# Optimization experiments

Hardware: AMD Instinct MI355X
Metric: run time of the kernel (lower is better)

## Reference

```python
import jax, jax.numpy as jnp
import numpy as np

D_MODEL = 1024
N_HEADS = 16
D_K = D_MODEL // N_HEADS
NEG = -1e9


def setup_inputs() -> dict:
    key = jax.random.key(0)
    ks = jax.random.split(key, 10)
    B, S = 4, 2048
    x = jax.random.normal(ks[0], (B, S, D_MODEL), dtype=jnp.float32)
    mask = jax.random.randint(ks[1], (B, S, S), 0, 2).astype(jnp.bool_)
    sc = 1.0 / np.sqrt(D_MODEL)
    Wq = jax.random.normal(ks[2], (D_MODEL, D_MODEL), dtype=jnp.float32) * sc
    bq = jnp.zeros((D_MODEL,), dtype=jnp.float32)
    Wk = jax.random.normal(ks[3], (D_MODEL, D_MODEL), dtype=jnp.float32) * sc
    bk = jnp.zeros((D_MODEL,), dtype=jnp.float32)
    Wv = jax.random.normal(ks[4], (D_MODEL, D_MODEL), dtype=jnp.float32) * sc
    bv = jnp.zeros((D_MODEL,), dtype=jnp.float32)
    Wo = jax.random.normal(ks[5], (D_MODEL, D_MODEL), dtype=jnp.float32) * sc
    bo = jnp.zeros((D_MODEL,), dtype=jnp.float32)
    return {"x": x, "mask": mask, "Wq": Wq, "bq": bq, "Wk": Wk, "bk": bk,
            "Wv": Wv, "bv": bv, "Wo": Wo, "bo": bo}


def _split_heads(t, B, S):
    # [B,S,d_model] -> [B,H,S,d_k]
    return t.reshape(B, S, N_HEADS, D_K).transpose(0, 2, 1, 3)


def reference(x, mask, Wq, bq, Wk, bk, Wv, bv, Wo, bo):
    B, S, _ = x.shape
    Q = _split_heads(x @ Wq + bq, B, S)
    K = _split_heads(x @ Wk + bk, B, S)
    V = _split_heads(x @ Wv + bv, B, S)
    scale = jnp.sqrt(jnp.float32(D_K))
    scores = jnp.einsum('bhqd,bhkd->bhqk', Q, K) / scale
    scores = jnp.where(mask[:, None, :, :], jnp.float32(NEG), scores)
    attn = jax.nn.softmax(scores, axis=-1)
    ctx = jnp.einsum('bhqk,bhkd->bhqd', attn, V)
    ctx = ctx.transpose(0, 2, 1, 3).reshape(B, S, D_MODEL)
    return ctx @ Wo + bo
```

## Files before the change

kernel.cpp:

```cpp
#include <hip/hip_runtime.h>

#define D_MODEL 1024
#define N_HEADS 16
#define D_K     64
#define BATCH   4
#define SEQ     2048
#define MROWS   (BATCH * SEQ)
#define QSCALE  0.18033688011112042f

typedef __bf16 bf16x8 __attribute__((ext_vector_type(8)));
typedef float  f32x4  __attribute__((ext_vector_type(4)));
typedef float  f32x16 __attribute__((ext_vector_type(16)));
typedef unsigned short ushort8 __attribute__((ext_vector_type(8)));
typedef unsigned short ushort4v __attribute__((ext_vector_type(4)));

#if __has_builtin(__builtin_amdgcn_exp2f)
#define EXP2F(x) __builtin_amdgcn_exp2f(x)
#else
#define EXP2F(x) exp2f(x)
#endif

__device__ inline unsigned short f2bf(float f) {
    union { float f; unsigned int u; } v; v.f = f;
    unsigned int u = v.u;
    unsigned int r = (u + 0x7fffu + ((u >> 16) & 1u)) >> 16;
    return (unsigned short)r;
}

__device__ inline void load_lds16(const void* g, void* l) {
    __builtin_amdgcn_global_load_lds(
        (const __attribute__((address_space(1))) unsigned int*)g,
        (__attribute__((address_space(3))) unsigned int*)l, 16, 0, 0);
}

__global__ __launch_bounds__(256) void wprep(const float* __restrict__ Wq,
                                             const float* __restrict__ Wk,
                                             const float* __restrict__ Wv,
                                             const float* __restrict__ Wo,
                                             unsigned short* __restrict__ wt) {
    __shared__ __align__(16) unsigned short t[64][65];
    int w  = blockIdx.z;
    const float* W = (w == 0) ? Wq : (w == 1) ? Wk : (w == 2) ? Wv : Wo;
    int k0 = blockIdx.x * 64, n0 = blockIdx.y * 64;
    int tid = threadIdx.x;
    int nl = tid & 63, kq = tid >> 6;
#pragma unroll
    for (int i = 0; i < 16; i++) {
        int kl = kq * 16 + i;
        t[kl][nl] = f2bf(W[(size_t)(k0 + kl) * D_MODEL + n0 + nl]);
    }
    __syncthreads();
    unsigned short* out = wt + (size_t)w * D_MODEL * D_MODEL;
#pragma unroll
    for (int p = 0; p < 2; p++) {
        int nrow = p * 32 + (tid >> 3);
        int c8   = (tid & 7) * 8;
        ushort8 o;
#pragma unroll
        for (int j = 0; j < 8; j++) o[j] = t[c8 + j][nrow];
        *reinterpret_cast<ushort8*>(out + (size_t)(n0 + nrow) * D_MODEL + k0 + c8) = o;
    }
}

__global__ __launch_bounds__(256) void xprep(const float4* __restrict__ x,
                                             unsigned short* __restrict__ xb) {
    int i = blockIdx.x * 256 + threadIdx.x;
    float4 v = x[i];
    ushort4v o;
    o[0] = f2bf(v.x); o[1] = f2bf(v.y); o[2] = f2bf(v.z); o[3] = f2bf(v.w);
    *reinterpret_cast<ushort4v*>(xb + (size_t)i * 4) = o;
}

__global__ __launch_bounds__(256) void mprep(const int* __restrict__ mask,
                                             unsigned long long* __restrict__ mb) {
    int row = blockIdx.x;
    int tid = threadIdx.x;
    int wv  = tid >> 6;
#pragma unroll
    for (int w = 0; w < 8; w++) {
        int col = w * 256 + tid;
        int mval = mask[(size_t)row * SEQ + col];
        unsigned long long bits = __ballot(mval != 0);
        if ((tid & 63) == 0) mb[(size_t)row * 32 + w * 4 + wv] = bits;
    }
}

__global__ __launch_bounds__(256) void qkv_gemm(const unsigned short* __restrict__ xb,
                                                const unsigned short* __restrict__ wt,
                                                const float* __restrict__ bq,
                                                const float* __restrict__ bk,
                                                const float* __restrict__ bvv,
                                                unsigned short* __restrict__ qb,
                                                unsigned short* __restrict__ kb,
                                                unsigned short* __restrict__ vt) {
    __shared__ __align__(16) unsigned short lds_a[128 * 32];
    __shared__ __align__(16) unsigned short lds_b[128 * 32];
    int tid = threadIdx.x;
    int wave = tid >> 6, lane = tid & 63;
    int c = lane & 15, g = lane >> 4;
    int wave_m = (wave & 1) * 64, wave_n = (wave >> 1) * 64;
    int nblk = blockIdx.x * 128, mblk = blockIdx.y * 128;

    int oct0 = wave * 128 + lane, oct1 = oct0 + 64;
    int ra0 = oct0 >> 2, ga0 = ((oct0 & 3) ^ (ra0 & 3)) * 8;
    int ra1 = oct1 >> 2, ga1 = ((oct1 & 3) ^ (ra1 & 3)) * 8;
    const unsigned short* pa0 = xb + (size_t)(mblk + ra0) * D_MODEL + ga0;
    const unsigned short* pa1 = xb + (size_t)(mblk + ra1) * D_MODEL + ga1;
    const unsigned short* pb0 = wt + (size_t)(nblk + ra0) * D_MODEL + ga0;
    const unsigned short* pb1 = wt + (size_t)(nblk + ra1) * D_MODEL + ga1;
    unsigned short* la0 = lds_a + wave * 1024;
    unsigned short* la1 = la0 + 512;
    unsigned short* lb0 = lds_b + wave * 1024;
    unsigned short* lb1 = lb0 + 512;

    int aoff[4], boff[4];
#pragma unroll
    for (int mi = 0; mi < 4; mi++) {
        int row = wave_m + mi * 16 + c;
        aoff[mi] = (row * 4 + (g ^ (row & 3))) * 16;
    }
#pragma unroll
    for (int ni = 0; ni < 4; ni++) {
        int row = wave_n + ni * 16 + c;
        boff[ni] = (row * 4 + (g ^ (row & 3))) * 16;
    }

    f32x4 acc[4][4];
#pragma unroll
    for (int mi = 0; mi < 4; mi++)
#pragma unroll
        for (int ni = 0; ni < 4; ni++) acc[mi][ni] = f32x4{0.f, 0.f, 0.f, 0.f};

    for (int k0 = 0; k0 < D_MODEL; k0 += 32) {
        load_lds16(pa0 + k0, la0);
        load_lds16(pa1 + k0, la1);
        load_lds16(pb0 + k0, lb0);
        load_lds16(pb1 + k0, lb1);
        __syncthreads();
        bf16x8 af[4], bfr[4];
#pragma unroll
        for (int mi = 0; mi < 4; mi++)
            af[mi] = *reinterpret_cast<const bf16x8*>(reinterpret_cast<const char*>(lds_a) + aoff[mi]);
#pragma unroll
        for (int ni = 0; ni < 4; ni++)
            bfr[ni] = *reinterpret_cast<const bf16x8*>(reinterpret_cast<const char*>(lds_b) + boff[ni]);
#pragma unroll
        for (int mi = 0; mi < 4; mi++)
#pragma unroll
            for (int ni = 0; ni < 4; ni++)
                acc[mi][ni] = __builtin_amdgcn_mfma_f32_16x16x32_bf16(af[mi], bfr[ni], acc[mi][ni], 0, 0, 0);
        __syncthreads();
    }

    int nb = nblk + wave_n;
    int wsel = nb >> 10;
    int h = (nb >> 6) & 15;
    int dk0 = nb & 63;
    int mglob = mblk + wave_m;
    int b = mglob >> 11;
    int s0 = mglob & (SEQ - 1);
    size_t bh = (size_t)(b * N_HEADS + h);
    const float* bias = (wsel == 0) ? bq : (wsel == 1) ? bk : bvv;
    int nn = nb & (D_MODEL - 1);
    float bval[4];
#pragma unroll
    for (int ni = 0; ni < 4; ni++) bval[ni] = bias[nn + ni * 16 + c];
    float oscale = (wsel == 0) ? QSCALE : 1.0f;

    if (wsel < 2) {
        unsigned short* outp = wsel ? kb : qb;
#pragma unroll
        for (int mi = 0; mi < 4; mi++)
#pragma unroll
            for (int ni = 0; ni < 4; ni++) {
                int dk = dk0 + ni * 16 + c;
#pragma unroll
                for (int r = 0; r < 4; r++) {
                    int s = s0 + mi * 16 + g * 4 + r;
                    outp[(bh * SEQ + s) * 64 + dk] = f2bf((acc[mi][ni][r] + bval[ni]) * oscale);
                }
            }
    } else {
#pragma unroll
        for (int mi = 0; mi < 4; mi++)
#pragma unroll
            for (int ni = 0; ni < 4; ni++) {
                int dk = dk0 + ni * 16 + c;
                int s = s0 + mi * 16 + g * 4;
                ushort4v o;
#pragma unroll
                for (int r = 0; r < 4; r++) o[r] = f2bf(acc[mi][ni][r] + bval[ni]);
                *reinterpret_cast<ushort4v*>(vt + (bh * 64 + dk) * SEQ + s) = o;
            }
    }
}

__global__ __launch_bounds__(128) void attn(const unsigned short* __restrict__ qb,
                                            const unsigned short* __restrict__ kb,
                                            const unsigned short* __restrict__ vt,
                                            const unsigned long long* __restrict__ mb,
                                            unsigned short* __restrict__ ctx) {
    __shared__ __align__(16) unsigned char smem[25088];
    unsigned short* lk = (unsigned short*)smem;
    unsigned short* lv = (unsigned short*)(smem + 8192);
    unsigned int*  lpw = (unsigned int*)(smem + 16384);

    int tid = threadIdx.x;
    int wave = tid >> 6, lane = tid & 63;
    int q31 = lane & 31, hi = lane >> 5;
    int bh = blockIdx.x >> 5;
    int q0 = (blockIdx.x & 31) * 64 + wave * 32;
    int b = bh >> 4, h = bh & 15;
    const unsigned short* qbase = qb + (size_t)bh * SEQ * 64;
    const unsigned short* kbase = kb + (size_t)bh * SEQ * 64;
    const unsigned short* vbase = vt + (size_t)bh * 64 * SEQ;
    const unsigned long long* mp = mb + ((size_t)b * SEQ + q0 + q31) * 32;

    bf16x8 qf[4];
    {
        const unsigned short* qr = qbase + (size_t)(q0 + q31) * 64 + hi * 8;
#pragma unroll
        for (int c = 0; c < 4; c++)
            qf[c] = *reinterpret_cast<const bf16x8*>(qr + c * 16);
    }

    int srow = lane >> 3;
    int soct = (lane & 7) ^ srow;
    const unsigned short* ksrc[4];
    const unsigned short* vsrc[4];
    unsigned short* klb[4];
    unsigned short* vlb[4];
#pragma unroll
    for (int i = 0; i < 4; i++) {
        int rbase = 16 * i + 8 * wave;
        ksrc[i] = kbase + (size_t)(rbase + srow) * 64 + soct * 8;
        vsrc[i] = vbase + (size_t)(rbase + srow) * SEQ + soct * 8;
        klb[i] = lk + rbase * 64;
        vlb[i] = lv + rbase * 64;
    }

    int kofs[2][4];
#pragma unroll
    for (int s = 0; s < 2; s++)
#pragma unroll
        for (int c = 0; c < 4; c++)
            kofs[s][c] = (32 * s + q31) * 128 + (((hi + 2 * c) ^ (q31 & 7)) * 16);

    unsigned int* pw = lpw + wave * 1088 + q31 * 34 + 2 * hi;
    const unsigned int* prd = lpw + wave * 1088 + q31 * 34 + 4 * hi;

    float lsum = 0.f;
    f32x16 po[2];
#pragma unroll
    for (int i = 0; i < 16; i++) { po[0][i] = 0.f; po[1][i] = 0.f; }

    for (int it = 0; it < SEQ / 64; it++) {
#pragma unroll
        for (int i = 0; i < 4; i++) {
            load_lds16(ksrc[i] + it * 4096, klb[i]);
            load_lds16(vsrc[i] + it * 64, vlb[i]);
        }
        unsigned long long w64 = mp[it];
        __syncthreads();

        const char* lkb = (const char*)lk;
        const char* lvb = (const char*)lv;

        f32x16 sq[2];
#pragma unroll
        for (int i = 0; i < 16; i++) { sq[0][i] = 0.f; sq[1][i] = 0.f; }
#pragma unroll
        for (int c = 0; c < 4; c++) {
            sq[0] = __builtin_amdgcn_mfma_f32_32x32x16_bf16(
                *reinterpret_cast<const bf16x8*>(lkb + kofs[0][c]), qf[c], sq[0], 0, 0, 0);
            sq[1] = __builtin_amdgcn_mfma_f32_32x32x16_bf16(
                *reinterpret_cast<const bf16x8*>(lkb + kofs[1][c]), qf[c], sq[1], 0, 0, 0);
        }

#pragma unroll
        for (int s = 0; s < 2; s++) {
            unsigned int wt = ~(unsigned int)(w64 >> (32 * s));
#pragma unroll
            for (int j = 0; j < 4; j++) {
                unsigned int nj = wt >> (8 * j + 4 * hi);
                unsigned int t0, t1, t2, t3;
                {
                    float p = EXP2F(sq[s][4 * j + 0]);
                    unsigned int m = (unsigned int)((int)(nj << 31) >> 31);
                    t0 = __float_as_uint(p) & m; lsum += __uint_as_float(t0);
                }
                {
                    float p = EXP2F(sq[s][4 * j + 1]);
                    unsigned int m = (unsigned int)((int)(nj << 30) >> 31);
                    t1 = __float_as_uint(p) & m; lsum += __uint_as_float(t1);
                }
                {
                    float p = EXP2F(sq[s][4 * j + 2]);
                    unsigned int m = (unsigned int)((int)(nj << 29) >> 31);
                    t2 = __float_as_uint(p) & m; lsum += __uint_as_float(t2);
                }
                {
                    float p = EXP2F(sq[s][4 * j + 3]);
                    unsigned int m = (unsigned int)((int)(nj << 28) >> 31);
                    t3 = __float_as_uint(p) & m; lsum += __uint_as_float(t3);
                }
                uint2 u;
                u.x = (t0 >> 16) | (t1 & 0xFFFF0000u);
                u.y = (t2 >> 16) | (t3 & 0xFFFF0000u);
                *reinterpret_cast<uint2*>(pw + 16 * s + 4 * j) = u;
            }
        }

#pragma unroll
        for (int c = 0; c < 4; c++) {
            union { bf16x8 v; uint4 u; } pb;
            uint2 b0 = *reinterpret_cast<const uint2*>(prd + 8 * c);
            uint2 b1 = *reinterpret_cast<const uint2*>(prd + 8 * c + 2);
            pb.u = make_uint4(b0.x, b0.y, b1.x, b1.y);
            po[0] = __builtin_amdgcn_mfma_f32_32x32x16_bf16(
                *reinterpret_cast<const bf16x8*>(lvb + kofs[0][c]), pb.v, po[0], 0, 0, 0);
            po[1] = __builtin_amdgcn_mfma_f32_32x32x16_bf16(
                *reinterpret_cast<const bf16x8*>(lvb + kofs[1][c]), pb.v, po[1], 0, 0, 0);
        }
        __syncthreads();
    }

    lsum += __shfl_xor(lsum, 32);
    float invr = 1.f / lsum;

    unsigned int* ob = (unsigned int*)smem + wave * 1152 + q31 * 36 + 2 * hi;
#pragma unroll
    for (int t = 0; t < 2; t++)
#pragma unroll
        for (int j = 0; j < 4; j++) {
            unsigned int w0 = (unsigned int)f2bf(po[t][4 * j + 0] * invr)
                            | ((unsigned int)f2bf(po[t][4 * j + 1] * invr) << 16);
            unsigned int w1 = (unsigned int)f2bf(po[t][4 * j + 2] * invr)
                            | ((unsigned int)f2bf(po[t][4 * j + 3] * invr) << 16);
            uint2 u; u.x = w0; u.y = w1;
            *reinterpret_cast<uint2*>(ob + 16 * t + 4 * j) = u;
        }

    const unsigned int* obase = (const unsigned int*)smem + wave * 1152;
    size_t crow = (size_t)b * SEQ + q0;
#pragma unroll
    for (int i = 0; i < 4; i++) {
        int qq = i * 8 + (lane >> 3);
        int oo = lane & 7;
        uint4 v = *reinterpret_cast<const uint4*>(obase + qq * 36 + oo * 4);
        *reinterpret_cast<uint4*>(ctx + (crow + qq) * D_MODEL + h * 64 + oo * 8) = v;
    }
}

__global__ __launch_bounds__(256) void oproj(const unsigned short* __restrict__ ctx,
                                             const unsigned short* __restrict__ wt,
                                             const float* __restrict__ bo,
                                             float* __restrict__ out) {
    __shared__ __align__(16) unsigned short lds_a[128 * 32];
    __shared__ __align__(16) unsigned short lds_b[128 * 32];
    int tid = threadIdx.x;
    int wave = tid >> 6, lane = tid & 63;
    int c = lane & 15, g = lane >> 4;
    int wave_m = (wave & 1) * 64, wave_n = (wave >> 1) * 64;
    int nblk = blockIdx.x * 128, mblk = blockIdx.y * 128;
    const unsigned short* wo = wt + (size_t)3 * D_MODEL * D_MODEL;

    int oct0 = wave * 128 + lane, oct1 = oct0 + 64;
    int ra0 = oct0 >> 2, ga0 = ((oct0 & 3) ^ (ra0 & 3)) * 8;
    int ra1 = oct1 >> 2, ga1 = ((oct1 & 3) ^ (ra1 & 3)) * 8;
    const unsigned short* pa0 = ctx + (size_t)(mblk + ra0) * D_MODEL + ga0;
    const unsigned short* pa1 = ctx + (size_t)(mblk + ra1) * D_MODEL + ga1;
    const unsigned short* pb0 = wo + (size_t)(nblk + ra0) * D_MODEL + ga0;
    const unsigned short* pb1 = wo + (size_t)(nblk + ra1) * D_MODEL + ga1;
    unsigned short* la0 = lds_a + wave * 1024;
    unsigned short* la1 = la0 + 512;
    unsigned short* lb0 = lds_b + wave * 1024;
    unsigned short* lb1 = lb0 + 512;

    int aoff[4], boff[4];
#pragma unroll
    for (int mi = 0; mi < 4; mi++) {
        int row = wave_m + mi * 16 + c;
        aoff[mi] = (row * 4 + (g ^ (row & 3))) * 16;
    }
#pragma unroll
    for (int ni = 0; ni < 4; ni++) {
        int row = wave_n + ni * 16 + c;
        boff[ni] = (row * 4 + (g ^ (row & 3))) * 16;
    }

    f32x4 acc[4][4];
#pragma unroll
    for (int mi = 0; mi < 4; mi++)
#pragma unroll
        for (int ni = 0; ni < 4; ni++) acc[mi][ni] = f32x4{0.f, 0.f, 0.f, 0.f};

    for (int k0 = 0; k0 < D_MODEL; k0 += 32) {
        load_lds16(pa0 + k0, la0);
        load_lds16(pa1 + k0, la1);
        load_lds16(pb0 + k0, lb0);
        load_lds16(pb1 + k0, lb1);
        __syncthreads();
        bf16x8 af[4], bfr[4];
#pragma unroll
        for (int mi = 0; mi < 4; mi++)
            af[mi] = *reinterpret_cast<const bf16x8*>(reinterpret_cast<const char*>(lds_a) + aoff[mi]);
#pragma unroll
        for (int ni = 0; ni < 4; ni++)
            bfr[ni] = *reinterpret_cast<const bf16x8*>(reinterpret_cast<const char*>(lds_b) + boff[ni]);
#pragma unroll
        for (int mi = 0; mi < 4; mi++)
#pragma unroll
            for (int ni = 0; ni < 4; ni++)
                acc[mi][ni] = __builtin_amdgcn_mfma_f32_16x16x32_bf16(af[mi], bfr[ni], acc[mi][ni], 0, 0, 0);
        __syncthreads();
    }

    float bval[4];
#pragma unroll
    for (int ni = 0; ni < 4; ni++) bval[ni] = bo[nblk + wave_n + ni * 16 + c];
#pragma unroll
    for (int mi = 0; mi < 4; mi++)
#pragma unroll
        for (int ni = 0; ni < 4; ni++) {
            int n = nblk + wave_n + ni * 16 + c;
#pragma unroll
            for (int r = 0; r < 4; r++) {
                int m = mblk + wave_m + mi * 16 + g * 4 + r;
                out[(size_t)m * D_MODEL + n] = acc[mi][ni][r] + bval[ni];
            }
        }
}

extern "C" void kernel_launch(void* const* d_in, const int* in_sizes, int n_in,
                              void* d_out, int out_size, void* d_ws, size_t ws_size,
                              hipStream_t stream) {
    const float* x    = (const float*)d_in[0];
    const int*   mask = (const int*)d_in[1];
    const float* Wq = (const float*)d_in[2];
    const float* bq = (const float*)d_in[3];
    const float* Wk = (const float*)d_in[4];
    const float* bk = (const float*)d_in[5];
    const float* Wv = (const float*)d_in[6];
    const float* bv = (const float*)d_in[7];
    const float* Wo = (const float*)d_in[8];
    const float* bo = (const float*)d_in[9];
    float* out = (float*)d_out;

    char* ws = (char*)d_ws;
    const size_t MB = 1024 * 1024;
    unsigned short* wt  = (unsigned short*)(ws + 0 * MB);
    unsigned short* xb  = (unsigned short*)(ws + 8 * MB);
    unsigned short* qb  = (unsigned short*)(ws + 24 * MB);
    unsigned short* kb  = (unsigned short*)(ws + 40 * MB);
    unsigned short* vt  = (unsigned short*)(ws + 56 * MB);
    unsigned short* ctx = (unsigned short*)(ws + 72 * MB);
    unsigned long long* mb = (unsigned long long*)(ws + 88 * MB);

    wprep<<<dim3(16, 16, 4), 256, 0, stream>>>(Wq, Wk, Wv, Wo, wt);
    xprep<<<dim3(MROWS * D_MODEL / 4 / 256), 256, 0, stream>>>((const float4*)x, xb);
    mprep<<<dim3(MROWS), 256, 0, stream>>>(mask, mb);
    qkv_gemm<<<dim3(24, 64), 256, 0, stream>>>(xb, wt, bq, bk, bv, qb, kb, vt);
    attn<<<dim3(2048), 128, 0, stream>>>(qb, kb, vt, mb, ctx);
    oproj<<<dim3(8, 64), 256, 0, stream>>>(ctx, wt, bo, out);
}
```

Before: 411.5 us.

## Process 64 query rows per wave in attention to reuse K/V tiles

```diff
diff --git a/kernel.cpp b/kernel.cpp
--- a/kernel.cpp
+++ b/kernel.cpp
@@ -195,33 +195,35 @@
     }
 }
 
-__global__ __launch_bounds__(128) void attn(const unsigned short* __restrict__ qb,
-                                            const unsigned short* __restrict__ kb,
-                                            const unsigned short* __restrict__ vt,
-                                            const unsigned long long* __restrict__ mb,
-                                            unsigned short* __restrict__ ctx) {
-    __shared__ __align__(16) unsigned char smem[25088];
+__global__ __launch_bounds__(128, 2) void attn(const unsigned short* __restrict__ qb,
+                                               const unsigned short* __restrict__ kb,
+                                               const unsigned short* __restrict__ vt,
+                                               const unsigned long long* __restrict__ mb,
+                                               unsigned short* __restrict__ ctx) {
+    __shared__ __align__(16) unsigned char smem[36864];
     unsigned short* lk = (unsigned short*)smem;
     unsigned short* lv = (unsigned short*)(smem + 8192);
-    unsigned int*  lpw = (unsigned int*)(smem + 16384);
+    unsigned int*  lpA = (unsigned int*)(smem + 16384);
 
     int tid = threadIdx.x;
     int wave = tid >> 6, lane = tid & 63;
     int q31 = lane & 31, hi = lane >> 5;
-    int bh = blockIdx.x >> 5;
-    int q0 = (blockIdx.x & 31) * 64 + wave * 32;
+    int bh = blockIdx.x >> 4;
+    int q0 = (blockIdx.x & 15) * 128 + wave * 64;
     int b = bh >> 4, h = bh & 15;
     const unsigned short* qbase = qb + (size_t)bh * SEQ * 64;
     const unsigned short* kbase = kb + (size_t)bh * SEQ * 64;
     const unsigned short* vbase = vt + (size_t)bh * 64 * SEQ;
-    const unsigned long long* mp = mb + ((size_t)b * SEQ + q0 + q31) * 32;
-
-    bf16x8 qf[4];
-    {
-        const unsigned short* qr = qbase + (size_t)(q0 + q31) * 64 + hi * 8;
+    const unsigned long long* mp0 = mb + ((size_t)b * SEQ + q0 + q31) * 32;
+    const unsigned long long* mp1 = mp0 + 1024;
+
+    bf16x8 qf[2][4];
+#pragma unroll
+    for (int t = 0; t < 2; t++) {
+        const unsigned short* qr = qbase + (size_t)(q0 + 32 * t + q31) * 64 + hi * 8;
 #pragma unroll
         for (int c = 0; c < 4; c++)
-            qf[c] = *reinterpret_cast<const bf16x8*>(qr + c * 16);
+            qf[t][c] = *reinterpret_cast<const bf16x8*>(qr + c * 16);
     }
 
     int srow = lane >> 3;
@@ -246,13 +248,15 @@
         for (int c = 0; c < 4; c++)
             kofs[s][c] = (32 * s + q31) * 128 + (((hi + 2 * c) ^ (q31 & 7)) * 16);
 
-    unsigned int* pw = lpw + wave * 1088 + q31 * 34 + 2 * hi;
-    const unsigned int* prd = lpw + wave * 1088 + q31 * 34 + 4 * hi;
-
-    float lsum = 0.f;
-    f32x16 po[2];
-#pragma unroll
-    for (int i = 0; i < 16; i++) { po[0][i] = 0.f; po[1][i] = 0.f; }
+    unsigned int* lp = lpA + wave * 2560 + q31 * 20;
+
+    float lsum[2] = {0.f, 0.f};
+    f32x16 po[2][2];
+#pragma unroll
+    for (int i = 0; i < 16; i++) {
+        po[0][0][i] = 0.f; po[0][1][i] = 0.f;
+        po[1][0][i] = 0.f; po[1][1][i] = 0.f;
+    }
 
     for (int it = 0; it < SEQ / 64; it++) {
 #pragma unroll
@@ -260,95 +264,109 @@
             load_lds16(ksrc[i] + it * 4096, klb[i]);
             load_lds16(vsrc[i] + it * 64, vlb[i]);
         }
-        unsigned long long w64 = mp[it];
+        unsigned long long w64[2];
+        w64[0] = mp0[it];
+        w64[1] = mp1[it];
         __syncthreads();
 
         const char* lkb = (const char*)lk;
         const char* lvb = (const char*)lv;
 
-        f32x16 sq[2];
-#pragma unroll
-        for (int i = 0; i < 16; i++) { sq[0][i] = 0.f; sq[1][i] = 0.f; }
-#pragma unroll
-        for (int c = 0; c < 4; c++) {
-            sq[0] = __builtin_amdgcn_mfma_f32_32x32x16_bf16(
-                *reinterpret_cast<const bf16x8*>(lkb + kofs[0][c]), qf[c], sq[0], 0, 0, 0);
-            sq[1] = __builtin_amdgcn_mfma_f32_32x32x16_bf16(
-                *reinterpret_cast<const bf16x8*>(lkb + kofs[1][c]), qf[c], sq[1], 0, 0, 0);
+#pragma unroll
+        for (int s = 0; s < 2; s++) {
+            f32x16 sq[2];
+#pragma unroll
+            for (int i = 0; i < 16; i++) { sq[0][i] = 0.f; sq[1][i] = 0.f; }
+#pragma unroll
+            for (int c = 0; c < 4; c++) {
+                bf16x8 kf = *reinterpret_cast<const bf16x8*>(lkb + kofs[s][c]);
+                sq[0] = __builtin_amdgcn_mfma_f32_32x32x16_bf16(kf, qf[0][c], sq[0], 0, 0, 0);
+                sq[1] = __builtin_amdgcn_mfma_f32_32x32x16_bf16(kf, qf[1][c], sq[1], 0, 0, 0);
+            }
+#pragma unroll
+            for (int t = 0; t < 2; t++) {
+                unsigned int wt_ = ~(unsigned int)(w64[t] >> (32 * s));
+                unsigned int* pw = lp + (t * 2 + s) * 640;
+#pragma unroll
+                for (int j = 0; j < 4; j++) {
+                    unsigned int nj = wt_ >> (8 * j + 4 * hi);
+                    unsigned int t0, t1, t2, t3;
+                    {
+                        float p = EXP2F(sq[t][4 * j + 0]);
+                        unsigned int m = (unsigned int)((int)(nj << 31) >> 31);
+                        t0 = __float_as_uint(p) & m; lsum[t] += __uint_as_float(t0);
+                    }
+                    {
+                        float p = EXP2F(sq[t][4 * j + 1]);
+                        unsigned int m = (unsigned int)((int)(nj << 30) >> 31);
+                        t1 = __float_as_uint(p) & m; lsum[t] += __uint_as_float(t1);
+                    }
+                    {
+                        float p = EXP2F(sq[t][4 * j + 2]);
+                        unsigned int m = (unsigned int)((int)(nj << 29) >> 31);
+                        t2 = __float_as_uint(p) & m; lsum[t] += __uint_as_float(t2);
+                    }
+                    {
+                        float p = EXP2F(sq[t][4 * j + 3]);
+                        unsigned int m = (unsigned int)((int)(nj << 28) >> 31);
+                        t3 = __float_as_uint(p) & m; lsum[t] += __uint_as_float(t3);
+                    }
+                    uint2 u;
+                    u.x = (t0 >> 16) | (t1 & 0xFFFF0000u);
+                    u.y = (t2 >> 16) | (t3 & 0xFFFF0000u);
+                    *reinterpret_cast<uint2*>(pw + 4 * j + 2 * hi) = u;
+                }
+            }
+#pragma unroll
+            for (int cp = 0; cp < 2; cp++) {
+                int c = 2 * s + cp;
+                union { bf16x8 v; uint4 u; } pb0, pb1;
+                pb0.u = *reinterpret_cast<const uint4*>(lp + (0 * 2 + s) * 640 + 8 * cp + 4 * hi);
+                pb1.u = *reinterpret_cast<const uint4*>(lp + (1 * 2 + s) * 640 + 8 * cp + 4 * hi);
+#pragma unroll
+                for (int so = 0; so < 2; so++) {
+                    bf16x8 vf = *reinterpret_cast<const bf16x8*>(lvb + kofs[so][c]);
+                    po[0][so] = __builtin_amdgcn_mfma_f32_32x32x16_bf16(vf, pb0.v, po[0][so], 0, 0, 0);
+                    po[1][so] = __builtin_amdgcn_mfma_f32_32x32x16_bf16(vf, pb1.v, po[1][so], 0, 0, 0);
+                }
+            }
         }
-
-#pragma unroll
-        for (int s = 0; s < 2; s++) {
-            unsigned int wt = ~(unsigned int)(w64 >> (32 * s));
+        __syncthreads();
+    }
+
+    float inv[2];
+#pragma unroll
+    for (int t = 0; t < 2; t++) {
+        lsum[t] += __shfl_xor(lsum[t], 32);
+        inv[t] = 1.f / lsum[t];
+    }
+
+    unsigned int* ob = (unsigned int*)(smem + wave * 8192);
+    int csw = 4 * (q31 & 7);
+#pragma unroll
+    for (int t = 0; t < 2; t++) {
+        unsigned int* obr = ob + (32 * t + q31) * 32;
+#pragma unroll
+        for (int so = 0; so < 2; so++)
 #pragma unroll
             for (int j = 0; j < 4; j++) {
-                unsigned int nj = wt >> (8 * j + 4 * hi);
-                unsigned int t0, t1, t2, t3;
-                {
-                    float p = EXP2F(sq[s][4 * j + 0]);
-                    unsigned int m = (unsigned int)((int)(nj << 31) >> 31);
-                    t0 = __float_as_uint(p) & m; lsum += __uint_as_float(t0);
-                }
-                {
-                    float p = EXP2F(sq[s][4 * j + 1]);
-                    unsigned int m = (unsigned int)((int)(nj << 30) >> 31);
-                    t1 = __float_as_uint(p) & m; lsum += __uint_as_float(t1);
-                }
-                {
-                    float p = EXP2F(sq[s][4 * j + 2]);
-                    unsigned int m = (unsigned int)((int)(nj << 29) >> 31);
-                    t2 = __float_as_uint(p) & m; lsum += __uint_as_float(t2);
-                }
-                {
-                    float p = EXP2F(sq[s][4 * j + 3]);
-                    unsigned int m = (unsigned int)((int)(nj << 28) >> 31);
-                    t3 = __float_as_uint(p) & m; lsum += __uint_as_float(t3);
-                }
-                uint2 u;
-                u.x = (t0 >> 16) | (t1 & 0xFFFF0000u);
-                u.y = (t2 >> 16) | (t3 & 0xFFFF0000u);
-                *reinterpret_cast<uint2*>(pw + 16 * s + 4 * j) = u;
-            }
-        }
-
-#pragma unroll
-        for (int c = 0; c < 4; c++) {
-            union { bf16x8 v; uint4 u; } pb;
-            uint2 b0 = *reinterpret_cast<const uint2*>(prd + 8 * c);
-            uint2 b1 = *reinterpret_cast<const uint2*>(prd + 8 * c + 2);
-            pb.u = make_uint4(b0.x, b0.y, b1.x, b1.y);
-            po[0] = __builtin_amdgcn_mfma_f32_32x32x16_bf16(
-                *reinterpret_cast<const bf16x8*>(lvb + kofs[0][c]), pb.v, po[0], 0, 0, 0);
-            po[1] = __builtin_amdgcn_mfma_f32_32x32x16_bf16(
-                *reinterpret_cast<const bf16x8*>(lvb + kofs[1][c]), pb.v, po[1], 0, 0, 0);
-        }
-        __syncthreads();
-    }
-
-    lsum += __shfl_xor(lsum, 32);
-    float invr = 1.f / lsum;
-
-    unsigned int* ob = (unsigned int*)smem + wave * 1152 + q31 * 36 + 2 * hi;
-#pragma unroll
-    for (int t = 0; t < 2; t++)
-#pragma unroll
-        for (int j = 0; j < 4; j++) {
-            unsigned int w0 = (unsigned int)f2bf(po[t][4 * j + 0] * invr)
-                            | ((unsigned int)f2bf(po[t][4 * j + 1] * invr) << 16);
-            unsigned int w1 = (unsigned int)f2bf(po[t][4 * j + 2] * invr)
-                            | ((unsigned int)f2bf(po[t][4 * j + 3] * invr) << 16);
-            uint2 u; u.x = w0; u.y = w1;
-            *reinterpret_cast<uint2*>(ob + 16 * t + 4 * j) = u;
-        }
-
-    const unsigned int* obase = (const unsigned int*)smem + wave * 1152;
+                unsigned int w0 = (unsigned int)f2bf(po[t][so][4 * j + 0] * inv[t])
+                                | ((unsigned int)f2bf(po[t][so][4 * j + 1] * inv[t]) << 16);
+                unsigned int w1 = (unsigned int)f2bf(po[t][so][4 * j + 2] * inv[t])
+                                | ((unsigned int)f2bf(po[t][so][4 * j + 3] * inv[t]) << 16);
+                int d = (16 * so + 4 * j + 2 * hi) ^ csw;
+                uint2 u; u.x = w0; u.y = w1;
+                *reinterpret_cast<uint2*>(obr + d) = u;
+            }
+    }
+    __builtin_amdgcn_s_waitcnt(0);
     size_t crow = (size_t)b * SEQ + q0;
-#pragma unroll
-    for (int i = 0; i < 4; i++) {
-        int qq = i * 8 + (lane >> 3);
-        int oo = lane & 7;
-        uint4 v = *reinterpret_cast<const uint4*>(obase + qq * 36 + oo * 4);
-        *reinterpret_cast<uint4*>(ctx + (crow + qq) * D_MODEL + h * 64 + oo * 8) = v;
+    int o = lane & 7, rl = lane >> 3;
+#pragma unroll
+    for (int i = 0; i < 8; i++) {
+        int r = 8 * i + rl;
+        uint4 v = *reinterpret_cast<const uint4*>(ob + r * 32 + 4 * (o ^ (r & 7)));
+        *reinterpret_cast<uint4*>(ctx + (crow + r) * D_MODEL + h * 64 + o * 8) = v;
     }
 }
 
@@ -461,6 +479,6 @@
     xprep<<<dim3(MROWS * D_MODEL / 4 / 256), 256, 0, stream>>>((const float4*)x, xb);
     mprep<<<dim3(MROWS), 256, 0, stream>>>(mask, mb);
     qkv_gemm<<<dim3(24, 64), 256, 0, stream>>>(xb, wt, bq, bk, bv, qb, kb, vt);
-    attn<<<dim3(2048), 128, 0, stream>>>(qb, kb, vt, mb, ctx);
+    attn<<<dim3(1024), 128, 0, stream>>>(qb, kb, vt, mb, ctx);
     oproj<<<dim3(8, 64), 256, 0, stream>>>(ctx, wt, bo, out);
 }
```

After: 376.8 us. -8.4%, faster.
